# Kernel tuning notes

Hardware: AMD Instinct MI355X
Metric: run time of the kernel (lower is better)

## Reference

```python
import jax, jax.numpy as jnp
import numpy as np

N, E, HID, HEADS, EDIM = 32768, 262144, 64, 4, 3
C = HID  # per-head out channels (concat=False -> mean over heads)


def setup_inputs() -> dict:
    key = jax.random.key(0)
    ks = jax.random.split(key, 24)
    g = lambda k, shape, s=1.0: jax.random.normal(k, shape, jnp.float32) * s
    s_lin = 1.0 / np.sqrt(HID)
    s_edge = 1.0 / np.sqrt(EDIM)
    s_att = 1.0 / np.sqrt(C)
    inp = {
        "t": jnp.zeros((1,), jnp.float32),
        "h": g(ks[0], (N, HID)),
        "edge_index": jax.random.randint(ks[1], (2, E), 0, N, jnp.int32),
        "edge_attr": g(ks[2], (E, EDIM)),
        "W1": g(ks[3], (HID, HEADS * C), s_lin),
        "We1": g(ks[4], (EDIM, HEADS * C), s_edge),
        "att_src1": g(ks[5], (HEADS, C), s_att),
        "att_dst1": g(ks[6], (HEADS, C), s_att),
        "att_edge1": g(ks[7], (HEADS, C), s_att),
        "b1": jnp.zeros((C,), jnp.float32),
        "ln_g1": jnp.ones((HID,), jnp.float32),
        "ln_b1": jnp.zeros((HID,), jnp.float32),
        # last GAT layer's lin weight is scaled by 0.1 in __init__
        "W2": g(ks[8], (HID, HEADS * C), s_lin) * 0.1,
        "We2": g(ks[9], (EDIM, HEADS * C), s_edge),
        "att_src2": g(ks[10], (HEADS, C), s_att),
        "att_dst2": g(ks[11], (HEADS, C), s_att),
        "att_edge2": g(ks[12], (HEADS, C), s_att),
        "b2": jnp.zeros((C,), jnp.float32),
        "ln_g2": jnp.ones((HID,), jnp.float32),
        "ln_b2": jnp.zeros((HID,), jnp.float32),
    }
    return inp


def _gat_layer(z, src, dst, edge_attr, W, We, a_src, a_dst, a_edge, b):
    # PyG GATConv(edge_dim>0, concat=False, add_self_loops=False), eval mode (no dropout)
    x = (z @ W).reshape(-1, HEADS, C)                      # [N,H,C]
    alpha_s = jnp.einsum("nhc,hc->nh", x, a_src)           # [N,H]
    alpha_d = jnp.einsum("nhc,hc->nh", x, a_dst)           # [N,H]
    e = (edge_attr @ We).reshape(-1, HEADS, C)             # [E,H,C]
    alpha_e = jnp.einsum("ehc,hc->eh", e, a_edge)          # [E,H]
    logit = jax.nn.leaky_relu(alpha_s[src] + alpha_d[dst] + alpha_e, 0.2)  # [E,H]
    # segment softmax over incoming edges of each destination node
    m = jax.lax.stop_gradient(jax.ops.segment_max(logit, dst, num_segments=N))
    ex = jnp.exp(logit - m[dst])
    denom = jax.ops.segment_sum(ex, dst, num_segments=N)
    alpha = ex / (denom[dst] + 1e-16)                      # [E,H]
    msg = x[src] * alpha[..., None]                        # [E,H,C] gather + weight
    out = jax.ops.segment_sum(msg, dst, num_segments=N)    # [N,H,C] scatter-add
    return out.mean(axis=1) + b                            # head mean + bias -> [N,C]


def _layernorm(x, g, b, eps=1e-5):
    mu = x.mean(-1, keepdims=True)
    var = ((x - mu) ** 2).mean(-1, keepdims=True)
    return (x - mu) * jax.lax.rsqrt(var + eps) * g + b


def reference(t, h, edge_index, edge_attr, W1, We1, att_src1, att_dst1, att_edge1, b1,
              ln_g1, ln_b1, W2, We2, att_src2, att_dst2, att_edge2, b2, ln_g2, ln_b2):
    del t  # autonomous ODE func: t unused
    src, dst = edge_index[0], edge_index[1]
    z = h
    z = jax.nn.silu(_layernorm(_gat_layer(z, src, dst, edge_attr, W1, We1, att_src1, att_dst1, att_edge1, b1), ln_g1, ln_b1))
    z = jax.nn.silu(_layernorm(_gat_layer(z, src, dst, edge_attr, W2, We2, att_src2, att_dst2, att_edge2, b2), ln_g2, ln_b2))
    return z
```

## Files before the change

### kernel.cpp

```cpp
#include <hip/hip_runtime.h>
#include <math.h>

#define HIDDEN 64
#define HEADS 4
#define HC 256
#define CAP 64

typedef __attribute__((ext_vector_type(8))) short short8;
typedef __attribute__((ext_vector_type(4))) float f32x4;

__device__ __forceinline__ unsigned short f2bf(float f) {
    unsigned int u = __float_as_uint(f);
    u += 0x7fffu + ((u >> 16) & 1u);
    return (unsigned short)(u >> 16);
}

__global__ __launch_bounds__(256) void k_prep(const float* __restrict__ h,
                                              const float* __restrict__ W1f,
                                              const float* __restrict__ W2f,
                                              const float* __restrict__ We1,
                                              const float* __restrict__ at1,
                                              const float* __restrict__ We2,
                                              const float* __restrict__ at2,
                                              ushort* __restrict__ zb,
                                              ushort* __restrict__ wt1,
                                              ushort* __restrict__ wt2,
                                              float* __restrict__ wr,
                                              int* __restrict__ counts) {
    int t = threadIdx.x, b = blockIdx.x;
    if (b < 2048) {
        int i = b * 256 + t;
        float4 v = ((const float4*)h)[i];
        ushort4 o;
        o.x = f2bf(v.x); o.y = f2bf(v.y); o.z = f2bf(v.z); o.w = f2bf(v.w);
        ((ushort4*)zb)[i] = o;
    } else if (b < 2112) {
        int j = (b - 2048) * 256 + t;
        int c = j >> 6, k = j & 63;
        wt1[j] = f2bf(W1f[k * HC + c]);
        wt2[j] = f2bf(W2f[k * HC + c]);
    } else if (b == 2112) {
        int wv = t >> 6, lane = t & 63;
#pragma unroll
        for (int it = 0; it < 6; ++it) {
            int comb = wv + it * 4;
            int layer = comb / 12;
            int dh = comb % 12;
            int d = dh >> 2, hh = dh & 3;
            const float* We = layer ? We2 : We1;
            const float* at = layer ? at2 : at1;
            float v = We[d * HC + hh * HIDDEN + lane] * at[hh * HIDDEN + lane];
            for (int o = 32; o > 0; o >>= 1) v += __shfl_down(v, o);
            if (lane == 0) wr[layer * 16 + d * HEADS + hh] = v;
        }
    } else {
        counts[(b - 2113) * 256 + t] = 0;
    }
}

__global__ __launch_bounds__(256) void k_bucket(const int* __restrict__ dst,
                                                const int* __restrict__ src,
                                                const float* __restrict__ ea,
                                                const float* __restrict__ wr,
                                                int* __restrict__ counts,
                                                int* __restrict__ sb,
                                                float* __restrict__ a1b,
                                                float* __restrict__ a2b, int E) {
    int e = blockIdx.x * blockDim.x + threadIdx.x;
    if (e >= E) return;
    int d = dst[e];
    int c = atomicAdd(&counts[d], 1);
    if (c >= CAP) return;
    size_t slot = (size_t)d * CAP + c;
    sb[slot] = src[e];
    float a0 = ea[e * 3 + 0];
    float a1 = ea[e * 3 + 1];
    float a2 = ea[e * 3 + 2];
    float o1[4], o2[4];
#pragma unroll
    for (int hh = 0; hh < 4; ++hh) {
        o1[hh] = a0 * wr[hh] + a1 * wr[4 + hh] + a2 * wr[8 + hh];
        o2[hh] = a0 * wr[16 + hh] + a1 * wr[20 + hh] + a2 * wr[24 + hh];
    }
    *(float4*)&a1b[slot * 4] = make_float4(o1[0], o1[1], o1[2], o1[3]);
    *(float4*)&a2b[slot * 4] = make_float4(o2[0], o2[1], o2[2], o2[3]);
}

__global__ __launch_bounds__(256) void k_tmfma(const ushort* __restrict__ zb,
                                               const ushort* __restrict__ wt,
                                               const float* __restrict__ asw,
                                               const float* __restrict__ adw,
                                               ushort* __restrict__ xb,
                                               float* __restrict__ as_,
                                               float* __restrict__ ad_) {
    int wave = threadIdx.x >> 6, lane = threadIdx.x & 63;
    int q = lane & 15, quad = lane >> 4;
    int row0 = blockIdx.x * 64 + wave * 16;

    const ushort* zrow = zb + (size_t)(row0 + q) * 64 + quad * 8;
    short8 a0 = *(const short8*)(zrow);
    short8 a1 = *(const short8*)(zrow + 32);

#pragma unroll
    for (int h = 0; h < 4; ++h) {
        float vs[4] = {0.f, 0.f, 0.f, 0.f};
        float vd[4] = {0.f, 0.f, 0.f, 0.f};
#pragma unroll
        for (int nt = 0; nt < 4; ++nt) {
            int col0 = h * 64 + nt * 16;
            const ushort* wrow = wt + (size_t)(col0 + q) * 64 + quad * 8;
            short8 b0 = *(const short8*)(wrow);
            short8 b1 = *(const short8*)(wrow + 32);
            f32x4 acc = {0.f, 0.f, 0.f, 0.f};
            acc = __builtin_amdgcn_mfma_f32_16x16x32_bf16(a0, b0, acc, 0, 0, 0);
            acc = __builtin_amdgcn_mfma_f32_16x16x32_bf16(a1, b1, acc, 0, 0, 0);
            int c = col0 + q;
            float aw = asw[c], dw = adw[c];
#pragma unroll
            for (int r = 0; r < 4; ++r) {
                float v = acc[r];
                xb[(size_t)(row0 + quad * 4 + r) * HC + c] = f2bf(v);
                vs[r] += v * aw;
                vd[r] += v * dw;
            }
        }
#pragma unroll
        for (int o = 1; o < 16; o <<= 1) {
#pragma unroll
            for (int r = 0; r < 4; ++r) {
                vs[r] += __shfl_xor(vs[r], o);
                vd[r] += __shfl_xor(vd[r], o);
            }
        }
        if (q < 4) {
            int n = row0 + quad * 4 + q;
            as_[n * 4 + h] = vs[q];
            ad_[n * 4 + h] = vd[q];
        }
    }
}

__global__ __launch_bounds__(256) void k_aggregate(
        const ushort* __restrict__ xb, const float* __restrict__ aes,
        const int* __restrict__ sb, const int* __restrict__ counts,
        const float* __restrict__ as_, const float* __restrict__ ad_,
        const float* __restrict__ bias, const float* __restrict__ lng,
        const float* __restrict__ lnb, float* __restrict__ outf,
        ushort* __restrict__ outb, int N) {
    int lane = threadIdx.x & 63;
    int h = lane >> 4, sub = lane & 15;
    int e = sub & 1, g = sub >> 1;
    int wid = blockIdx.x * 4 + (threadIdx.x >> 6);
    int nwaves = gridDim.x * 4;

    float bs[8], gm[8], bt[8];
#pragma unroll
    for (int k = 0; k < 8; ++k) {
        bs[k] = bias[g * 8 + k];
        gm[k] = lng[g * 8 + k];
        bt[k] = lnb[g * 8 + k];
    }

    for (int n = wid; n < N; n += nwaves) {
        int deg = counts[n];
        if (deg > CAP) deg = CAP;
        int base = n * CAP;
        float ad4 = ad_[n * 4 + h];

        float ssum = 0.f;
        float acc[8];
#pragma unroll
        for (int k = 0; k < 8; ++k) acc[k] = 0.f;

        for (int cs = 0; cs < deg; cs += 16) {
            int idx = cs + sub;
            int s_sub = 0;
            float wgt = 0.f;
            if (idx < deg) {
                s_sub = sb[base + idx];
                float lg = as_[s_sub * 4 + h] + aes[(size_t)(base + idx) * 4 + h] + ad4;
                lg = (lg >= 0.f) ? lg : 0.2f * lg;
                wgt = __expf(lg);
            }
            ssum += wgt;

            int jb = deg - cs; if (jb > 16) jb = 16;
            for (int j4 = 0; j4 < jb; j4 += 4) {
                int sl0 = h * 16 + j4 + e;
                int sl1 = h * 16 + j4 + 2 + e;
                float w0 = __shfl(wgt, sl0);
                int s0 = __shfl(s_sub, sl0);
                float w1 = __shfl(wgt, sl1);
                int s1 = __shfl(s_sub, sl1);
                uint4 r0 = *(const uint4*)&xb[(size_t)s0 * HC + h * HIDDEN + g * 8];
                uint4 r1 = *(const uint4*)&xb[(size_t)s1 * HC + h * HIDDEN + g * 8];
                unsigned int u0[4] = {r0.x, r0.y, r0.z, r0.w};
                unsigned int u1[4] = {r1.x, r1.y, r1.z, r1.w};
#pragma unroll
                for (int k = 0; k < 4; ++k) {
                    acc[2 * k + 0] += w0 * __uint_as_float(u0[k] << 16);
                    acc[2 * k + 1] += w0 * __uint_as_float(u0[k] & 0xffff0000u);
                    acc[2 * k + 0] += w1 * __uint_as_float(u1[k] << 16);
                    acc[2 * k + 1] += w1 * __uint_as_float(u1[k] & 0xffff0000u);
                }
            }
        }
#pragma unroll
        for (int o = 1; o < 16; o <<= 1) ssum += __shfl_xor(ssum, o);
        float winv = 1.f / (ssum + 1e-16f);
#pragma unroll
        for (int k = 0; k < 8; ++k) acc[k] *= winv;
#pragma unroll
        for (int k = 0; k < 8; ++k) {
            acc[k] += __shfl_xor(acc[k], 1);
            acc[k] += __shfl_xor(acc[k], 16);
            acc[k] += __shfl_xor(acc[k], 32);
        }

        float u8[8], s1 = 0.f;
#pragma unroll
        for (int k = 0; k < 8; ++k) {
            u8[k] = acc[k] * 0.25f + bs[k];
            s1 += u8[k];
        }
#pragma unroll
        for (int o = 2; o < 16; o <<= 1) s1 += __shfl_xor(s1, o);
        float mu = s1 * (1.f / 64.f);
        float s2 = 0.f;
#pragma unroll
        for (int k = 0; k < 8; ++k) {
            float d = u8[k] - mu;
            s2 += d * d;
        }
#pragma unroll
        for (int o = 2; o < 16; o <<= 1) s2 += __shfl_xor(s2, o);
        float rstd = rsqrtf(s2 * (1.f / 64.f) + 1e-5f);
        float r[8];
#pragma unroll
        for (int k = 0; k < 8; ++k) {
            float y = (u8[k] - mu) * rstd * gm[k] + bt[k];
            r[k] = y / (1.f + __expf(-y));
        }
        if ((lane & 49) == 0) {
            if (outb) {
                uint4 pk;
                pk.x = (unsigned)f2bf(r[0]) | ((unsigned)f2bf(r[1]) << 16);
                pk.y = (unsigned)f2bf(r[2]) | ((unsigned)f2bf(r[3]) << 16);
                pk.z = (unsigned)f2bf(r[4]) | ((unsigned)f2bf(r[5]) << 16);
                pk.w = (unsigned)f2bf(r[6]) | ((unsigned)f2bf(r[7]) << 16);
                *(uint4*)&outb[(size_t)n * HIDDEN + g * 8] = pk;
            } else {
                float4* o4 = (float4*)&outf[(size_t)n * HIDDEN + g * 8];
                o4[0] = make_float4(r[0], r[1], r[2], r[3]);
                o4[1] = make_float4(r[4], r[5], r[6], r[7]);
            }
        }
    }
}


extern "C" void kernel_launch(void* const* d_in, const int* in_sizes, int n_in,
                              void* d_out, int out_size, void* d_ws, size_t ws_size,
                              hipStream_t stream) {
    const float* h   = (const float*)d_in[1];
    const int*   ei  = (const int*)d_in[2];
    const float* ea  = (const float*)d_in[3];
    const float* W1  = (const float*)d_in[4];
    const float* We1 = (const float*)d_in[5];
    const float* as1 = (const float*)d_in[6];
    const float* ad1 = (const float*)d_in[7];
    const float* ae1 = (const float*)d_in[8];
    const float* b1  = (const float*)d_in[9];
    const float* lg1 = (const float*)d_in[10];
    const float* lb1 = (const float*)d_in[11];
    const float* W2  = (const float*)d_in[12];
    const float* We2 = (const float*)d_in[13];
    const float* as2 = (const float*)d_in[14];
    const float* ad2 = (const float*)d_in[15];
    const float* ae2 = (const float*)d_in[16];
    const float* b2  = (const float*)d_in[17];
    const float* lg2 = (const float*)d_in[18];
    const float* lb2 = (const float*)d_in[19];

    const int N = in_sizes[1] / HIDDEN;
    const int E = in_sizes[2] / 2;
    const int* srcp = ei;
    const int* dstp = ei + E;

    char* w = (char*)d_ws;
    ushort* xb    = (ushort*)w; w += (size_t)N * HC * 2;
    ushort* zb    = (ushort*)w; w += (size_t)N * HIDDEN * 2;
    float* as_    = (float*)w;  w += (size_t)N * HEADS * 4;
    float* adv    = (float*)w;  w += (size_t)N * HEADS * 4;
    ushort* wt1   = (ushort*)w; w += 16384 * 2;
    ushort* wt2   = (ushort*)w; w += 16384 * 2;
    float* wr     = (float*)w;  w += 128;
    int* counts   = (int*)w;    w += (size_t)N * 4;
    int* sb       = (int*)w;    w += (size_t)N * CAP * 4;
    float* a1b    = (float*)w;  w += (size_t)N * CAP * 4 * 4;
    float* a2b    = (float*)w;  w += (size_t)N * CAP * 4 * 4;

    k_prep<<<2241, 256, 0, stream>>>(h, W1, W2, We1, ae1, We2, ae2,
                                     zb, wt1, wt2, wr, counts);
    k_bucket<<<(E + 255) / 256, 256, 0, stream>>>(dstp, srcp, ea, wr, counts,
                                                  sb, a1b, a2b, E);

    k_tmfma<<<N / 64, 256, 0, stream>>>(zb, wt1, as1, ad1, xb, as_, adv);
    k_aggregate<<<4096, 256, 0, stream>>>(xb, a1b, sb, counts, as_, adv,
                                          b1, lg1, lb1, nullptr, zb, N);
    k_tmfma<<<N / 64, 256, 0, stream>>>(zb, wt2, as2, ad2, xb, as_, adv);
    k_aggregate<<<4096, 256, 0, stream>>>(xb, a2b, sb, counts, as_, adv,
                                          b2, lg2, lb2, (float*)d_out, nullptr, N);
}
```

Measured before the change: 224.4 us.

## Aggregate raw features before projection, fold attention vectors into weights

Result: slower. 260.8 us (+16.3%).

```diff
diff --git a/kernel.cpp b/kernel.cpp
--- a/kernel.cpp
+++ b/kernel.cpp
@@ -22,10 +22,15 @@
                                               const float* __restrict__ at1,
                                               const float* __restrict__ We2,
                                               const float* __restrict__ at2,
+                                              const float* __restrict__ as1,
+                                              const float* __restrict__ ad1,
+                                              const float* __restrict__ as2,
+                                              const float* __restrict__ ad2,
                                               ushort* __restrict__ zb,
-                                              ushort* __restrict__ wt1,
-                                              ushort* __restrict__ wt2,
+                                              ushort* __restrict__ wtm1,
+                                              ushort* __restrict__ wtm2,
                                               float* __restrict__ wr,
+                                              float* __restrict__ wvec,
                                               int* __restrict__ counts) {
     int t = threadIdx.x, b = blockIdx.x;
     if (b < 2048) {
@@ -36,9 +41,10 @@
         ((ushort4*)zb)[i] = o;
     } else if (b < 2112) {
         int j = (b - 2048) * 256 + t;
-        int c = j >> 6, k = j & 63;
-        wt1[j] = f2bf(W1f[k * HC + c]);
-        wt2[j] = f2bf(W2f[k * HC + c]);
+        int c = j >> 8, k = j & 255;
+        int hh = k >> 6, d = k & 63;
+        wtm1[j] = f2bf(0.25f * W1f[d * HC + hh * HIDDEN + c]);
+        wtm2[j] = f2bf(0.25f * W2f[d * HC + hh * HIDDEN + c]);
     } else if (b == 2112) {
         int wv = t >> 6, lane = t & 63;
 #pragma unroll
@@ -53,8 +59,18 @@
             for (int o = 32; o > 0; o >>= 1) v += __shfl_down(v, o);
             if (lane == 0) wr[layer * 16 + d * HEADS + hh] = v;
         }
+    } else if (b < 2117) {
+        int blk = b - 2113;
+        int layer = blk >> 1, sd = blk & 1;
+        const float* W = layer ? W2f : W1f;
+        const float* at = layer ? (sd ? ad2 : as2) : (sd ? ad1 : as1);
+        int hh = t >> 6, d = t & 63;
+        float v = 0.f;
+        for (int c = 0; c < 64; ++c)
+            v += W[d * HC + hh * HIDDEN + c] * at[hh * HIDDEN + c];
+        wvec[layer * 512 + sd * 256 + hh * 64 + d] = v;
     } else {
-        counts[(b - 2113) * 256 + t] = 0;
+        counts[(b - 2117) * 256 + t] = 0;
     }
 }
 
@@ -86,174 +102,189 @@
     *(float4*)&a2b[slot * 4] = make_float4(o2[0], o2[1], o2[2], o2[3]);
 }
 
-__global__ __launch_bounds__(256) void k_tmfma(const ushort* __restrict__ zb,
-                                               const ushort* __restrict__ wt,
-                                               const float* __restrict__ asw,
-                                               const float* __restrict__ adw,
-                                               ushort* __restrict__ xb,
+__global__ __launch_bounds__(256) void k_alpha(const ushort* __restrict__ zb,
+                                               const float* __restrict__ wv,
                                                float* __restrict__ as_,
-                                               float* __restrict__ ad_) {
-    int wave = threadIdx.x >> 6, lane = threadIdx.x & 63;
-    int q = lane & 15, quad = lane >> 4;
-    int row0 = blockIdx.x * 64 + wave * 16;
-
-    const ushort* zrow = zb + (size_t)(row0 + q) * 64 + quad * 8;
-    short8 a0 = *(const short8*)(zrow);
-    short8 a1 = *(const short8*)(zrow + 32);
-
-#pragma unroll
-    for (int h = 0; h < 4; ++h) {
-        float vs[4] = {0.f, 0.f, 0.f, 0.f};
-        float vd[4] = {0.f, 0.f, 0.f, 0.f};
-#pragma unroll
-        for (int nt = 0; nt < 4; ++nt) {
-            int col0 = h * 64 + nt * 16;
-            const ushort* wrow = wt + (size_t)(col0 + q) * 64 + quad * 8;
-            short8 b0 = *(const short8*)(wrow);
-            short8 b1 = *(const short8*)(wrow + 32);
-            f32x4 acc = {0.f, 0.f, 0.f, 0.f};
-            acc = __builtin_amdgcn_mfma_f32_16x16x32_bf16(a0, b0, acc, 0, 0, 0);
-            acc = __builtin_amdgcn_mfma_f32_16x16x32_bf16(a1, b1, acc, 0, 0, 0);
-            int c = col0 + q;
-            float aw = asw[c], dw = adw[c];
-#pragma unroll
-            for (int r = 0; r < 4; ++r) {
-                float v = acc[r];
-                xb[(size_t)(row0 + quad * 4 + r) * HC + c] = f2bf(v);
-                vs[r] += v * aw;
-                vd[r] += v * dw;
-            }
-        }
-#pragma unroll
-        for (int o = 1; o < 16; o <<= 1) {
-#pragma unroll
-            for (int r = 0; r < 4; ++r) {
-                vs[r] += __shfl_xor(vs[r], o);
-                vd[r] += __shfl_xor(vd[r], o);
-            }
-        }
-        if (q < 4) {
-            int n = row0 + quad * 4 + q;
-            as_[n * 4 + h] = vs[q];
-            ad_[n * 4 + h] = vd[q];
-        }
-    }
-}
-
-__global__ __launch_bounds__(256) void k_aggregate(
-        const ushort* __restrict__ xb, const float* __restrict__ aes,
+                                               float* __restrict__ adv, int N) {
+    int n = blockIdx.x * 256 + threadIdx.x;
+    if (n >= N) return;
+    const uint4* zr = (const uint4*)(zb + (size_t)n * 64);
+    float s[4] = {0, 0, 0, 0}, d[4] = {0, 0, 0, 0};
+#pragma unroll
+    for (int j = 0; j < 8; ++j) {
+        uint4 z4 = zr[j];
+        unsigned u[4] = {z4.x, z4.y, z4.z, z4.w};
+#pragma unroll
+        for (int k = 0; k < 4; ++k) {
+            float lo = __uint_as_float(u[k] << 16);
+            float hi = __uint_as_float(u[k] & 0xffff0000u);
+            int c = j * 8 + 2 * k;
+#pragma unroll
+            for (int hh = 0; hh < 4; ++hh) {
+                s[hh] += lo * wv[hh * 64 + c] + hi * wv[hh * 64 + c + 1];
+                d[hh] += lo * wv[256 + hh * 64 + c] + hi * wv[256 + hh * 64 + c + 1];
+            }
+        }
+    }
+    *(float4*)&as_[n * 4] = make_float4(s[0], s[1], s[2], s[3]);
+    *(float4*)&adv[n * 4] = make_float4(d[0], d[1], d[2], d[3]);
+}
+
+__global__ __launch_bounds__(256) void k_aggz(
+        const ushort* __restrict__ zb, const float* __restrict__ aes,
         const int* __restrict__ sb, const int* __restrict__ counts,
         const float* __restrict__ as_, const float* __restrict__ ad_,
-        const float* __restrict__ bias, const float* __restrict__ lng,
-        const float* __restrict__ lnb, float* __restrict__ outf,
-        ushort* __restrict__ outb, int N) {
+        ushort* __restrict__ zagg, int N) {
     int lane = threadIdx.x & 63;
-    int h = lane >> 4, sub = lane & 15;
-    int e = sub & 1, g = sub >> 1;
+    int e = lane >> 3, g = lane & 7;
     int wid = blockIdx.x * 4 + (threadIdx.x >> 6);
     int nwaves = gridDim.x * 4;
-
-    float bs[8], gm[8], bt[8];
-#pragma unroll
-    for (int k = 0; k < 8; ++k) {
-        bs[k] = bias[g * 8 + k];
-        gm[k] = lng[g * 8 + k];
-        bt[k] = lnb[g * 8 + k];
-    }
 
     for (int n = wid; n < N; n += nwaves) {
         int deg = counts[n];
         if (deg > CAP) deg = CAP;
         int base = n * CAP;
-        float ad4 = ad_[n * 4 + h];
-
-        float ssum = 0.f;
-        float acc[8];
-#pragma unroll
-        for (int k = 0; k < 8; ++k) acc[k] = 0.f;
-
-        for (int cs = 0; cs < deg; cs += 16) {
-            int idx = cs + sub;
-            int s_sub = 0;
-            float wgt = 0.f;
+        float4 adv4 = *(const float4*)&ad_[n * 4];
+
+        float acc[4][8];
+        float ssum[4] = {0.f, 0.f, 0.f, 0.f};
+#pragma unroll
+        for (int hh = 0; hh < 4; ++hh)
+#pragma unroll
+            for (int k = 0; k < 8; ++k) acc[hh][k] = 0.f;
+
+        for (int cs = 0; cs < deg; cs += 8) {
+            int idx = cs + e;
+            int s = 0;
+            float w[4] = {0.f, 0.f, 0.f, 0.f};
             if (idx < deg) {
-                s_sub = sb[base + idx];
-                float lg = as_[s_sub * 4 + h] + aes[(size_t)(base + idx) * 4 + h] + ad4;
-                lg = (lg >= 0.f) ? lg : 0.2f * lg;
-                wgt = __expf(lg);
-            }
-            ssum += wgt;
-
-            int jb = deg - cs; if (jb > 16) jb = 16;
-            for (int j4 = 0; j4 < jb; j4 += 4) {
-                int sl0 = h * 16 + j4 + e;
-                int sl1 = h * 16 + j4 + 2 + e;
-                float w0 = __shfl(wgt, sl0);
-                int s0 = __shfl(s_sub, sl0);
-                float w1 = __shfl(wgt, sl1);
-                int s1 = __shfl(s_sub, sl1);
-                uint4 r0 = *(const uint4*)&xb[(size_t)s0 * HC + h * HIDDEN + g * 8];
-                uint4 r1 = *(const uint4*)&xb[(size_t)s1 * HC + h * HIDDEN + g * 8];
-                unsigned int u0[4] = {r0.x, r0.y, r0.z, r0.w};
-                unsigned int u1[4] = {r1.x, r1.y, r1.z, r1.w};
-#pragma unroll
-                for (int k = 0; k < 4; ++k) {
-                    acc[2 * k + 0] += w0 * __uint_as_float(u0[k] << 16);
-                    acc[2 * k + 1] += w0 * __uint_as_float(u0[k] & 0xffff0000u);
-                    acc[2 * k + 0] += w1 * __uint_as_float(u1[k] << 16);
-                    acc[2 * k + 1] += w1 * __uint_as_float(u1[k] & 0xffff0000u);
+                s = sb[base + idx];
+                float4 av = *(const float4*)&as_[s * 4];
+                float4 cv = *(const float4*)&aes[(size_t)(base + idx) * 4];
+                float lg;
+                lg = av.x + adv4.x + cv.x; lg = (lg >= 0.f) ? lg : 0.2f * lg; w[0] = __expf(lg);
+                lg = av.y + adv4.y + cv.y; lg = (lg >= 0.f) ? lg : 0.2f * lg; w[1] = __expf(lg);
+                lg = av.z + adv4.z + cv.z; lg = (lg >= 0.f) ? lg : 0.2f * lg; w[2] = __expf(lg);
+                lg = av.w + adv4.w + cv.w; lg = (lg >= 0.f) ? lg : 0.2f * lg; w[3] = __expf(lg);
+            }
+#pragma unroll
+            for (int hh = 0; hh < 4; ++hh) ssum[hh] += w[hh];
+            uint4 raw = *(const uint4*)&zb[(size_t)s * 64 + g * 8];
+            unsigned u[4] = {raw.x, raw.y, raw.z, raw.w};
+#pragma unroll
+            for (int k = 0; k < 4; ++k) {
+                float lo = __uint_as_float(u[k] << 16);
+                float hi = __uint_as_float(u[k] & 0xffff0000u);
+#pragma unroll
+                for (int hh = 0; hh < 4; ++hh) {
+                    acc[hh][2 * k + 0] += w[hh] * lo;
+                    acc[hh][2 * k + 1] += w[hh] * hi;
                 }
             }
         }
 #pragma unroll
-        for (int o = 1; o < 16; o <<= 1) ssum += __shfl_xor(ssum, o);
-        float winv = 1.f / (ssum + 1e-16f);
-#pragma unroll
-        for (int k = 0; k < 8; ++k) acc[k] *= winv;
-#pragma unroll
-        for (int k = 0; k < 8; ++k) {
-            acc[k] += __shfl_xor(acc[k], 1);
-            acc[k] += __shfl_xor(acc[k], 16);
-            acc[k] += __shfl_xor(acc[k], 32);
-        }
-
-        float u8[8], s1 = 0.f;
-#pragma unroll
-        for (int k = 0; k < 8; ++k) {
-            u8[k] = acc[k] * 0.25f + bs[k];
-            s1 += u8[k];
-        }
-#pragma unroll
-        for (int o = 2; o < 16; o <<= 1) s1 += __shfl_xor(s1, o);
-        float mu = s1 * (1.f / 64.f);
-        float s2 = 0.f;
-#pragma unroll
-        for (int k = 0; k < 8; ++k) {
-            float d = u8[k] - mu;
-            s2 += d * d;
-        }
-#pragma unroll
-        for (int o = 2; o < 16; o <<= 1) s2 += __shfl_xor(s2, o);
-        float rstd = rsqrtf(s2 * (1.f / 64.f) + 1e-5f);
-        float r[8];
-#pragma unroll
-        for (int k = 0; k < 8; ++k) {
-            float y = (u8[k] - mu) * rstd * gm[k] + bt[k];
-            r[k] = y / (1.f + __expf(-y));
-        }
-        if ((lane & 49) == 0) {
-            if (outb) {
+        for (int o = 8; o < 64; o <<= 1) {
+#pragma unroll
+            for (int hh = 0; hh < 4; ++hh) {
+                ssum[hh] += __shfl_xor(ssum[hh], o);
+#pragma unroll
+                for (int k = 0; k < 8; ++k)
+                    acc[hh][k] += __shfl_xor(acc[hh][k], o);
+            }
+        }
+        if (e == 0) {
+#pragma unroll
+            for (int hh = 0; hh < 4; ++hh) {
+                float winv = 1.f / (ssum[hh] + 1e-16f);
                 uint4 pk;
-                pk.x = (unsigned)f2bf(r[0]) | ((unsigned)f2bf(r[1]) << 16);
-                pk.y = (unsigned)f2bf(r[2]) | ((unsigned)f2bf(r[3]) << 16);
-                pk.z = (unsigned)f2bf(r[4]) | ((unsigned)f2bf(r[5]) << 16);
-                pk.w = (unsigned)f2bf(r[6]) | ((unsigned)f2bf(r[7]) << 16);
-                *(uint4*)&outb[(size_t)n * HIDDEN + g * 8] = pk;
-            } else {
-                float4* o4 = (float4*)&outf[(size_t)n * HIDDEN + g * 8];
-                o4[0] = make_float4(r[0], r[1], r[2], r[3]);
-                o4[1] = make_float4(r[4], r[5], r[6], r[7]);
-            }
+                pk.x = (unsigned)f2bf(acc[hh][0] * winv) | ((unsigned)f2bf(acc[hh][1] * winv) << 16);
+                pk.y = (unsigned)f2bf(acc[hh][2] * winv) | ((unsigned)f2bf(acc[hh][3] * winv) << 16);
+                pk.z = (unsigned)f2bf(acc[hh][4] * winv) | ((unsigned)f2bf(acc[hh][5] * winv) << 16);
+                pk.w = (unsigned)f2bf(acc[hh][6] * winv) | ((unsigned)f2bf(acc[hh][7] * winv) << 16);
+                *(uint4*)&zagg[(size_t)n * HC + hh * 64 + g * 8] = pk;
+            }
+        }
+    }
+}
+
+__global__ __launch_bounds__(256) void k_out(const ushort* __restrict__ zagg,
+                                             const ushort* __restrict__ wtm,
+                                             const float* __restrict__ bias,
+                                             const float* __restrict__ lng,
+                                             const float* __restrict__ lnb,
+                                             float* __restrict__ outf,
+                                             ushort* __restrict__ outb) {
+    int wave = threadIdx.x >> 6, lane = threadIdx.x & 63;
+    int q = lane & 15, quad = lane >> 4;
+    int row0 = blockIdx.x * 64 + wave * 16;
+
+    const ushort* arow = zagg + (size_t)(row0 + q) * HC + quad * 8;
+    short8 a[8];
+#pragma unroll
+    for (int ks = 0; ks < 8; ++ks) a[ks] = *(const short8*)(arow + ks * 32);
+
+    f32x4 acc[4];
+#pragma unroll
+    for (int nt = 0; nt < 4; ++nt) {
+        acc[nt] = (f32x4){0.f, 0.f, 0.f, 0.f};
+        const ushort* brow = wtm + (size_t)(nt * 16 + q) * HC + quad * 8;
+#pragma unroll
+        for (int ks = 0; ks < 8; ++ks) {
+            short8 bfr = *(const short8*)(brow + ks * 32);
+            acc[nt] = __builtin_amdgcn_mfma_f32_16x16x32_bf16(a[ks], bfr, acc[nt], 0, 0, 0);
+        }
+    }
+
+    float bs[4], gm[4], bt[4];
+#pragma unroll
+    for (int nt = 0; nt < 4; ++nt) {
+        bs[nt] = bias[nt * 16 + q];
+        gm[nt] = lng[nt * 16 + q];
+        bt[nt] = lnb[nt * 16 + q];
+    }
+    float u[4][4];
+#pragma unroll
+    for (int nt = 0; nt < 4; ++nt)
+#pragma unroll
+        for (int r = 0; r < 4; ++r) u[nt][r] = acc[nt][r] + bs[nt];
+
+    float s1[4];
+#pragma unroll
+    for (int r = 0; r < 4; ++r) s1[r] = u[0][r] + u[1][r] + u[2][r] + u[3][r];
+#pragma unroll
+    for (int o = 1; o < 16; o <<= 1)
+#pragma unroll
+        for (int r = 0; r < 4; ++r) s1[r] += __shfl_xor(s1[r], o);
+    float mu[4];
+#pragma unroll
+    for (int r = 0; r < 4; ++r) mu[r] = s1[r] * (1.f / 64.f);
+
+    float s2[4];
+#pragma unroll
+    for (int r = 0; r < 4; ++r) {
+        s2[r] = 0.f;
+#pragma unroll
+        for (int nt = 0; nt < 4; ++nt) {
+            float dd = u[nt][r] - mu[r];
+            s2[r] += dd * dd;
+        }
+    }
+#pragma unroll
+    for (int o = 1; o < 16; o <<= 1)
+#pragma unroll
+        for (int r = 0; r < 4; ++r) s2[r] += __shfl_xor(s2[r], o);
+
+#pragma unroll
+    for (int r = 0; r < 4; ++r) {
+        float rstd = rsqrtf(s2[r] * (1.f / 64.f) + 1e-5f);
+        int row = row0 + quad * 4 + r;
+#pragma unroll
+        for (int nt = 0; nt < 4; ++nt) {
+            float y = (u[nt][r] - mu[r]) * rstd * gm[nt] + bt[nt];
+            float res = y / (1.f + __expf(-y));
+            int col = nt * 16 + q;
+            if (outb) outb[(size_t)row * HIDDEN + col] = f2bf(res);
+            else outf[(size_t)row * HIDDEN + col] = res;
         }
     }
 }
@@ -288,27 +319,29 @@
     const int* dstp = ei + E;
 
     char* w = (char*)d_ws;
-    ushort* xb    = (ushort*)w; w += (size_t)N * HC * 2;
     ushort* zb    = (ushort*)w; w += (size_t)N * HIDDEN * 2;
+    ushort* zagg  = (ushort*)w; w += (size_t)N * HC * 2;
     float* as_    = (float*)w;  w += (size_t)N * HEADS * 4;
     float* adv    = (float*)w;  w += (size_t)N * HEADS * 4;
-    ushort* wt1   = (ushort*)w; w += 16384 * 2;
-    ushort* wt2   = (ushort*)w; w += 16384 * 2;
+    ushort* wtm1  = (ushort*)w; w += 16384 * 2;
+    ushort* wtm2  = (ushort*)w; w += 16384 * 2;
     float* wr     = (float*)w;  w += 128;
+    float* wvec   = (float*)w;  w += 1024 * 4;
     int* counts   = (int*)w;    w += (size_t)N * 4;
     int* sb       = (int*)w;    w += (size_t)N * CAP * 4;
     float* a1b    = (float*)w;  w += (size_t)N * CAP * 4 * 4;
     float* a2b    = (float*)w;  w += (size_t)N * CAP * 4 * 4;
 
-    k_prep<<<2241, 256, 0, stream>>>(h, W1, W2, We1, ae1, We2, ae2,
-                                     zb, wt1, wt2, wr, counts);
+    k_prep<<<2245, 256, 0, stream>>>(h, W1, W2, We1, ae1, We2, ae2,
+                                     as1, ad1, as2, ad2,
+                                     zb, wtm1, wtm2, wr, wvec, counts);
     k_bucket<<<(E + 255) / 256, 256, 0, stream>>>(dstp, srcp, ea, wr, counts,
                                                   sb, a1b, a2b, E);
 
-    k_tmfma<<<N / 64, 256, 0, stream>>>(zb, wt1, as1, ad1, xb, as_, adv);
-    k_aggregate<<<4096, 256, 0, stream>>>(xb, a1b, sb, counts, as_, adv,
-                                          b1, lg1, lb1, nullptr, zb, N);
-    k_tmfma<<<N / 64, 256, 0, stream>>>(zb, wt2, as2, ad2, xb, as_, adv);
-    k_aggregate<<<4096, 256, 0, stream>>>(xb, a2b, sb, counts, as_, adv,
-                                          b2, lg2, lb2, (float*)d_out, nullptr, N);
-}
+    k_alpha<<<N / 256, 256, 0, stream>>>(zb, wvec, as_, adv, N);
+    k_aggz<<<4096, 256, 0, stream>>>(zb, a1b, sb, counts, as_, adv, zagg, N);
+    k_out<<<N / 64, 256, 0, stream>>>(zagg, wtm1, b1, lg1, lb1, nullptr, zb);
+    k_alpha<<<N / 256, 256, 0, stream>>>(zb, wvec + 512, as_, adv, N);
+    k_aggz<<<4096, 256, 0, stream>>>(zb, a2b, sb, counts, as_, adv, zagg, N);
+    k_out<<<N / 64, 256, 0, stream>>>(zagg, wtm2, b2, lg2, lb2, (float*)d_out, nullptr);
+}
```

## Fuse edge bucketing into prep kernel and compute edge logits in aggregate

Applied to the files above, without the earlier changes.

Result: no change. 221.6 us, median of 2 (-1.2%).

```diff
diff --git a/kernel.cpp b/kernel.cpp
--- a/kernel.cpp
+++ b/kernel.cpp
@@ -15,31 +15,48 @@
     return (unsigned short)(u >> 16);
 }
 
-__global__ __launch_bounds__(256) void k_prep(const float* __restrict__ h,
-                                              const float* __restrict__ W1f,
-                                              const float* __restrict__ W2f,
-                                              const float* __restrict__ We1,
-                                              const float* __restrict__ at1,
-                                              const float* __restrict__ We2,
-                                              const float* __restrict__ at2,
-                                              ushort* __restrict__ zb,
-                                              ushort* __restrict__ wt1,
-                                              ushort* __restrict__ wt2,
-                                              float* __restrict__ wr,
-                                              int* __restrict__ counts) {
+__global__ __launch_bounds__(256) void k_fused(const int* __restrict__ dst,
+                                               const int* __restrict__ src,
+                                               const float* __restrict__ ea,
+                                               const float* __restrict__ h,
+                                               const float* __restrict__ W1f,
+                                               const float* __restrict__ W2f,
+                                               const float* __restrict__ We1,
+                                               const float* __restrict__ at1,
+                                               const float* __restrict__ We2,
+                                               const float* __restrict__ at2,
+                                               int* __restrict__ counts,
+                                               int* __restrict__ sb,
+                                               float* __restrict__ eab,
+                                               ushort* __restrict__ zb,
+                                               ushort* __restrict__ wt1,
+                                               ushort* __restrict__ wt2,
+                                               float* __restrict__ wr, int E) {
     int t = threadIdx.x, b = blockIdx.x;
-    if (b < 2048) {
-        int i = b * 256 + t;
+    if (b < 1024) {
+        int e = b * 256 + t;
+        if (e < E) {
+            int d = dst[e];
+            int c = atomicAdd(&counts[d], 1);
+            if (c < CAP) {
+                size_t slot = (size_t)d * CAP + c;
+                sb[slot] = src[e];
+                *(float4*)&eab[slot * 4] =
+                    make_float4(ea[e * 3 + 0], ea[e * 3 + 1], ea[e * 3 + 2], 0.f);
+            }
+        }
+    } else if (b < 3072) {
+        int i = (b - 1024) * 256 + t;
         float4 v = ((const float4*)h)[i];
         ushort4 o;
         o.x = f2bf(v.x); o.y = f2bf(v.y); o.z = f2bf(v.z); o.w = f2bf(v.w);
         ((ushort4*)zb)[i] = o;
-    } else if (b < 2112) {
-        int j = (b - 2048) * 256 + t;
+    } else if (b < 3136) {
+        int j = (b - 3072) * 256 + t;
         int c = j >> 6, k = j & 63;
         wt1[j] = f2bf(W1f[k * HC + c]);
         wt2[j] = f2bf(W2f[k * HC + c]);
-    } else if (b == 2112) {
+    } else {
         int wv = t >> 6, lane = t & 63;
 #pragma unroll
         for (int it = 0; it < 6; ++it) {
@@ -53,37 +70,7 @@
             for (int o = 32; o > 0; o >>= 1) v += __shfl_down(v, o);
             if (lane == 0) wr[layer * 16 + d * HEADS + hh] = v;
         }
-    } else {
-        counts[(b - 2113) * 256 + t] = 0;
     }
-}
-
-__global__ __launch_bounds__(256) void k_bucket(const int* __restrict__ dst,
-                                                const int* __restrict__ src,
-                                                const float* __restrict__ ea,
-                                                const float* __restrict__ wr,
-                                                int* __restrict__ counts,
-                                                int* __restrict__ sb,
-                                                float* __restrict__ a1b,
-                                                float* __restrict__ a2b, int E) {
-    int e = blockIdx.x * blockDim.x + threadIdx.x;
-    if (e >= E) return;
-    int d = dst[e];
-    int c = atomicAdd(&counts[d], 1);
-    if (c >= CAP) return;
-    size_t slot = (size_t)d * CAP + c;
-    sb[slot] = src[e];
-    float a0 = ea[e * 3 + 0];
-    float a1 = ea[e * 3 + 1];
-    float a2 = ea[e * 3 + 2];
-    float o1[4], o2[4];
-#pragma unroll
-    for (int hh = 0; hh < 4; ++hh) {
-        o1[hh] = a0 * wr[hh] + a1 * wr[4 + hh] + a2 * wr[8 + hh];
-        o2[hh] = a0 * wr[16 + hh] + a1 * wr[20 + hh] + a2 * wr[24 + hh];
-    }
-    *(float4*)&a1b[slot * 4] = make_float4(o1[0], o1[1], o1[2], o1[3]);
-    *(float4*)&a2b[slot * 4] = make_float4(o2[0], o2[1], o2[2], o2[3]);
 }
 
 __global__ __launch_bounds__(256) void k_tmfma(const ushort* __restrict__ zb,
@@ -141,9 +128,10 @@
 }
 
 __global__ __launch_bounds__(256) void k_aggregate(
-        const ushort* __restrict__ xb, const float* __restrict__ aes,
+        const ushort* __restrict__ xb, const float* __restrict__ eab,
         const int* __restrict__ sb, const int* __restrict__ counts,
         const float* __restrict__ as_, const float* __restrict__ ad_,
+        const float* __restrict__ wrl,
         const float* __restrict__ bias, const float* __restrict__ lng,
         const float* __restrict__ lnb, float* __restrict__ outf,
         ushort* __restrict__ outb, int N) {
@@ -153,6 +141,8 @@
     int wid = blockIdx.x * 4 + (threadIdx.x >> 6);
     int nwaves = gridDim.x * 4;
 
+    float w0 = wrl[h], w1 = wrl[4 + h], w2 = wrl[8 + h];
+
     float bs[8], gm[8], bt[8];
 #pragma unroll
     for (int k = 0; k < 8; ++k) {
@@ -178,7 +168,9 @@
             float wgt = 0.f;
             if (idx < deg) {
                 s_sub = sb[base + idx];
-                float lg = as_[s_sub * 4 + h] + aes[(size_t)(base + idx) * 4 + h] + ad4;
+                float4 av = *(const float4*)&eab[(size_t)(base + idx) * 4];
+                float lg = as_[s_sub * 4 + h] + ad4
+                         + av.x * w0 + av.y * w1 + av.z * w2;
                 lg = (lg >= 0.f) ? lg : 0.2f * lg;
                 wgt = __expf(lg);
             }
@@ -188,9 +180,9 @@
             for (int j4 = 0; j4 < jb; j4 += 4) {
                 int sl0 = h * 16 + j4 + e;
                 int sl1 = h * 16 + j4 + 2 + e;
-                float w0 = __shfl(wgt, sl0);
+                float q0 = __shfl(wgt, sl0);
                 int s0 = __shfl(s_sub, sl0);
-                float w1 = __shfl(wgt, sl1);
+                float q1 = __shfl(wgt, sl1);
                 int s1 = __shfl(s_sub, sl1);
                 uint4 r0 = *(const uint4*)&xb[(size_t)s0 * HC + h * HIDDEN + g * 8];
                 uint4 r1 = *(const uint4*)&xb[(size_t)s1 * HC + h * HIDDEN + g * 8];
@@ -198,10 +190,10 @@
                 unsigned int u1[4] = {r1.x, r1.y, r1.z, r1.w};
 #pragma unroll
                 for (int k = 0; k < 4; ++k) {
-                    acc[2 * k + 0] += w0 * __uint_as_float(u0[k] << 16);
-                    acc[2 * k + 1] += w0 * __uint_as_float(u0[k] & 0xffff0000u);
-                    acc[2 * k + 0] += w1 * __uint_as_float(u1[k] << 16);
-                    acc[2 * k + 1] += w1 * __uint_as_float(u1[k] & 0xffff0000u);
+                    acc[2 * k + 0] += q0 * __uint_as_float(u0[k] << 16);
+                    acc[2 * k + 1] += q0 * __uint_as_float(u0[k] & 0xffff0000u);
+                    acc[2 * k + 0] += q1 * __uint_as_float(u1[k] << 16);
+                    acc[2 * k + 1] += q1 * __uint_as_float(u1[k] & 0xffff0000u);
                 }
             }
         }
@@ -297,18 +289,17 @@
     float* wr     = (float*)w;  w += 128;
     int* counts   = (int*)w;    w += (size_t)N * 4;
     int* sb       = (int*)w;    w += (size_t)N * CAP * 4;
-    float* a1b    = (float*)w;  w += (size_t)N * CAP * 4 * 4;
-    float* a2b    = (float*)w;  w += (size_t)N * CAP * 4 * 4;
-
-    k_prep<<<2241, 256, 0, stream>>>(h, W1, W2, We1, ae1, We2, ae2,
-                                     zb, wt1, wt2, wr, counts);
-    k_bucket<<<(E + 255) / 256, 256, 0, stream>>>(dstp, srcp, ea, wr, counts,
-                                                  sb, a1b, a2b, E);
+    float* eab    = (float*)w;  w += (size_t)N * CAP * 4 * 4;
+
+    hipMemsetAsync(counts, 0, (size_t)N * 4, stream);
+    k_fused<<<3137, 256, 0, stream>>>(dstp, srcp, ea, h, W1, W2,
+                                      We1, ae1, We2, ae2,
+                                      counts, sb, eab, zb, wt1, wt2, wr, E);
 
     k_tmfma<<<N / 64, 256, 0, stream>>>(zb, wt1, as1, ad1, xb, as_, adv);
-    k_aggregate<<<4096, 256, 0, stream>>>(xb, a1b, sb, counts, as_, adv,
+    k_aggregate<<<4096, 256, 0, stream>>>(xb, eab, sb, counts, as_, adv, wr,
                                           b1, lg1, lb1, nullptr, zb, N);
     k_tmfma<<<N / 64, 256, 0, stream>>>(zb, wt2, as2, ad2, xb, as_, adv);
-    k_aggregate<<<4096, 256, 0, stream>>>(xb, a2b, sb, counts, as_, adv,
+    k_aggregate<<<4096, 256, 0, stream>>>(xb, eab, sb, counts, as_, adv, wr + 16,
                                           b2, lg2, lb2, (float*)d_out, nullptr, N);
 }
```
